# Kernel tuning notes

Measured on AMD Instinct MI355X. Metric: run time of the kernel, lower is better.

Reference implementation:

```python
import jax, jax.numpy as jnp
import numpy as np

BN_EPS = 1e-5
TAU = 1.0  # gumbel temperature

def setup_inputs() -> dict:
    key = jax.random.key(0)
    ks = jax.random.split(key, 6)
    B, O, F, H, HID = 32, 4096, 256, 8, 128
    x = jax.random.normal(ks[0], (B, O, F), dtype=jnp.float32)
    gumbel_noise = jax.random.gumbel(ks[1], (B, O, H), dtype=jnp.float32)
    W_in = jax.random.normal(ks[2], (F, HID), dtype=jnp.float32) * (1.0 / np.sqrt(F))
    b_in = jnp.zeros((HID,), jnp.float32)
    W_blk = jax.random.normal(ks[3], (HID, HID), dtype=jnp.float32) * (1.0 / np.sqrt(HID))
    b_blk = jnp.zeros((HID,), jnp.float32)
    bn_gamma = jnp.ones((HID,), jnp.float32)
    bn_beta = jnp.zeros((HID,), jnp.float32)
    W_fc = jax.random.normal(ks[4], (HID, H), dtype=jnp.float32) * (1.0 / np.sqrt(HID))
    b_fc = jnp.zeros((H,), jnp.float32)
    return {"x": x, "gumbel_noise": gumbel_noise, "W_in": W_in, "b_in": b_in,
            "W_blk": W_blk, "b_blk": b_blk, "bn_gamma": bn_gamma, "bn_beta": bn_beta,
            "W_fc": W_fc, "b_fc": b_fc}

def reference(x, gumbel_noise, W_in, b_in, W_blk, b_blk, bn_gamma, bn_beta, W_fc, b_fc):
    B, O, F = x.shape
    xf = x.reshape(B * O, F)
    # DynamicNetwork head: input linear + relu, one residual block (Linear+BN+ReLU), fc
    h = jax.nn.relu(xf @ W_in + b_in)  # (B*O, HID)
    z = h @ W_blk + b_blk
    mu = z.mean(axis=0)
    var = z.var(axis=0)  # biased var, matches BatchNorm training normalization
    z = (z - mu) * jax.lax.rsqrt(var + BN_EPS) * bn_gamma + bn_beta
    h = jax.nn.relu(z) + h  # residual
    logits = (h @ W_fc + b_fc).reshape(B, O, -1)  # (B, O, H)
    # mask out zero-norm observations
    mask = (jnp.linalg.norm(x, axis=2) != 0)[..., None].astype(x.dtype)  # (B, O, 1)
    logits = logits * mask
    # gumbel softmax over observation dim (soft)
    w = jax.nn.softmax((logits + gumbel_noise) / TAU, axis=1)  # (B, O, H)
    # weighted sum pooling: algebraically the repeat-multiply-sum in the original
    pooled = jnp.einsum('boh,bof->bhf', w, x)  # (B, H, F)
    return pooled.reshape(B, -1)  # (B, H*F)
```

## Files before the change

kernel.cpp:

```cpp
#include <hip/hip_runtime.h>
#include <hip/hip_bf16.h>
#include <math.h>

#define MB_ 131072
#define F_  256
#define HID_ 128
#define H_  8
#define O_  4096
#define B_  32

typedef __attribute__((ext_vector_type(8))) short short8;
typedef __attribute__((ext_vector_type(4))) float f32x4;

static __device__ __forceinline__ unsigned short f2bf(float f) {
    unsigned int u = __float_as_uint(f);
    unsigned int r = (u + 0x7fffu + ((u >> 16) & 1u)) >> 16;
    return (unsigned short)r;
}
static __device__ __forceinline__ float bf2f(unsigned short u) {
    return __uint_as_float(((unsigned int)u) << 16);
}
static __device__ __forceinline__ unsigned int pk2bf(float a, float b) {
    float2 f2; f2.x = a; f2.y = b;
    __hip_bfloat162 h = __float22bfloat162_rn(f2);
    union { __hip_bfloat162 h2; unsigned int u; } cv;
    cv.h2 = h;
    return cv.u;
}

__global__ __launch_bounds__(256) void k_prep(
    const float* __restrict__ W_in, const float* __restrict__ W_blk,
    unsigned short* __restrict__ Win_f, unsigned short* __restrict__ Wblk_f)
{
    const int idx = blockIdx.x * 256 + threadIdx.x;
    if (idx < 32768) {
        const int j = idx & 7, n = (idx >> 3) & 127, c = idx >> 10;
        Win_f[idx] = f2bf(W_in[(size_t)(c * 8 + j) * HID_ + n]);
    } else if (idx < 49152) {
        const int i2 = idx - 32768;
        const int j = i2 & 7, n = (i2 >> 3) & 127, c = i2 >> 10;
        Wblk_f[i2] = f2bf(W_blk[(size_t)(c * 8 + j) * HID_ + n]);
    }
}

__global__ __launch_bounds__(256, 3) void k_gemm1(
    const float* __restrict__ x, const unsigned short* __restrict__ Win_f,
    const float* __restrict__ b_in,
    unsigned short* __restrict__ h_f, float* __restrict__ mask_out)
{
    __shared__ __align__(16) unsigned short smem[128 * 136];
    unsigned short* a_s = smem;
    unsigned short* hb_s = smem;

    const int tid = threadIdx.x;
    const int R0 = blockIdx.x * 128;
    const int wave = tid >> 6;
    const int wrow = wave >> 1, wcol = wave & 1;
    const int lane = tid & 63;
    const int lm = lane & 15, quad = lane >> 4;
    const int srow = tid >> 3;
    const int sk = tid & 7;
    const int sq = sk >> 1, sh = sk & 1;

    f32x4 acc[4][4];
#pragma unroll
    for (int i = 0; i < 4; i++)
#pragma unroll
        for (int j = 0; j < 4; j++) acc[i][j] = (f32x4){0.f, 0.f, 0.f, 0.f};
    float ms[4] = {0.f, 0.f, 0.f, 0.f};

    const float* xrow = x + (size_t)(R0 + srow) * F_ + sk * 4;

    for (int kt = 0; kt < 8; kt++) {
#pragma unroll
        for (int p = 0; p < 4; p++) {
            const float4 v = *(const float4*)(xrow + kt * 32 + (size_t)(32 * p) * F_);
            ms[p] += v.x * v.x + v.y * v.y + v.z * v.z + v.w * v.w;
            uint2 w; w.x = pk2bf(v.x, v.y); w.y = pk2bf(v.z, v.w);
            *(uint2*)(&a_s[(sq * 132 + srow + 32 * p) * 8 + sh * 4]) = w;
        }
        __syncthreads();
        short8 af[4], bfr[4];
        const unsigned short* wf = Win_f + ((size_t)(kt * 4 + quad) * 128 + wcol * 64 + lm) * 8;
#pragma unroll
        for (int ni = 0; ni < 4; ni++)
            bfr[ni] = *(const short8*)(wf + ni * 16 * 8);
#pragma unroll
        for (int mi = 0; mi < 4; mi++)
            af[mi] = *(const short8*)(&a_s[(quad * 132 + wrow * 64 + mi * 16 + lm) * 8]);
#pragma unroll
        for (int mi = 0; mi < 4; mi++)
#pragma unroll
            for (int ni = 0; ni < 4; ni++)
                acc[mi][ni] = __builtin_amdgcn_mfma_f32_16x16x32_bf16(af[mi], bfr[ni], acc[mi][ni], 0, 0, 0);
        __syncthreads();
    }

#pragma unroll
    for (int p = 0; p < 4; p++) {
        float s = ms[p];
        s += __shfl_down(s, 4, 8);
        s += __shfl_down(s, 2, 8);
        s += __shfl_down(s, 1, 8);
        if (sk == 0) mask_out[R0 + srow + 32 * p] = (s != 0.f) ? 1.f : 0.f;
    }

    {
        float bcol[4];
#pragma unroll
        for (int ni = 0; ni < 4; ni++) bcol[ni] = b_in[wcol * 64 + ni * 16 + lm];
#pragma unroll
        for (int mi = 0; mi < 4; mi++)
#pragma unroll
            for (int r = 0; r < 4; r++) {
                const int row = wrow * 64 + mi * 16 + quad * 4 + r;
#pragma unroll
                for (int ni = 0; ni < 4; ni++) {
                    const int col = wcol * 64 + ni * 16 + lm;
                    hb_s[row * 136 + col] = f2bf(fmaxf(acc[mi][ni][r] + bcol[ni], 0.f));
                }
            }
    }
    __syncthreads();

    unsigned short* hf = h_f + (size_t)blockIdx.x * 16384;
#pragma unroll
    for (int i = 0; i < 8; i++) {
        const int idx = i * 256 + tid;
        const int c = idx >> 7, row = idx & 127;
        const short8 v = *(const short8*)(&hb_s[row * 136 + c * 8]);
        *(short8*)(hf + (size_t)idx * 8) = v;
    }
}

__global__ __launch_bounds__(256, 4) void k_gemm2stats(
    const unsigned short* __restrict__ h_f, const unsigned short* __restrict__ Wblk_f,
    const float* __restrict__ b_blk,
    float* __restrict__ sumP, float* __restrict__ sumsqP)
{
    __shared__ float csum_s[128], csumsq_s[128];
    const int tid = threadIdx.x;
    const int wave = tid >> 6;
    const int wrow = wave >> 1, wcol = wave & 1;
    const int lane = tid & 63;
    const int lm = lane & 15, quad = lane >> 4;

    if (tid < 128) { csum_s[tid] = 0.f; csumsq_s[tid] = 0.f; }
    __syncthreads();

    const unsigned short* hf = h_f + (size_t)blockIdx.x * 16384;

    f32x4 acc[4][4];
#pragma unroll
    for (int i = 0; i < 4; i++)
#pragma unroll
        for (int j = 0; j < 4; j++) acc[i][j] = (f32x4){0.f, 0.f, 0.f, 0.f};
#pragma unroll
    for (int kt = 0; kt < 4; kt++) {
        short8 af[4], bfr[4];
        const unsigned short* wf2 = Wblk_f + ((size_t)(kt * 4 + quad) * 128 + wcol * 64 + lm) * 8;
#pragma unroll
        for (int ni = 0; ni < 4; ni++)
            bfr[ni] = *(const short8*)(wf2 + ni * 16 * 8);
#pragma unroll
        for (int mi = 0; mi < 4; mi++)
            af[mi] = *(const short8*)(hf + ((size_t)(kt * 4 + quad) * 128 + wrow * 64 + mi * 16 + lm) * 8);
#pragma unroll
        for (int mi = 0; mi < 4; mi++)
#pragma unroll
            for (int ni = 0; ni < 4; ni++)
                acc[mi][ni] = __builtin_amdgcn_mfma_f32_16x16x32_bf16(af[mi], bfr[ni], acc[mi][ni], 0, 0, 0);
    }

    float bcol[4];
#pragma unroll
    for (int ni = 0; ni < 4; ni++) bcol[ni] = b_blk[wcol * 64 + ni * 16 + lm];
    float s_c[4] = {0.f, 0.f, 0.f, 0.f}, ss_c[4] = {0.f, 0.f, 0.f, 0.f};
#pragma unroll
    for (int mi = 0; mi < 4; mi++)
#pragma unroll
        for (int r = 0; r < 4; r++)
#pragma unroll
            for (int ni = 0; ni < 4; ni++) {
                const float zv = acc[mi][ni][r] + bcol[ni];
                s_c[ni] += zv;
                ss_c[ni] += zv * zv;
            }
#pragma unroll
    for (int ni = 0; ni < 4; ni++) {
        float s = s_c[ni], ss = ss_c[ni];
        s  += __shfl_xor(s, 16);  s  += __shfl_xor(s, 32);
        ss += __shfl_xor(ss, 16); ss += __shfl_xor(ss, 32);
        if (quad == 0) {
            atomicAdd(&csum_s[wcol * 64 + ni * 16 + lm], s);
            atomicAdd(&csumsq_s[wcol * 64 + ni * 16 + lm], ss);
        }
    }
    __syncthreads();
    if (tid < 128) {
        sumP[(size_t)blockIdx.x * 128 + tid] = csum_s[tid];
        sumsqP[(size_t)blockIdx.x * 128 + tid] = csumsq_s[tid];
    }
}

__global__ __launch_bounds__(256) void k_bnfin(
    const float* __restrict__ sumP, const float* __restrict__ sumsqP,
    const float* __restrict__ gamma, const float* __restrict__ beta,
    float* __restrict__ scale, float* __restrict__ shift)
{
    const int c = blockIdx.x;
    const int tid = threadIdx.x;
    float s = 0.f, ss = 0.f;
    for (int i = tid; i < 1024; i += 256) {
        s  += sumP[(size_t)i * 128 + c];
        ss += sumsqP[(size_t)i * 128 + c];
    }
#pragma unroll
    for (int off = 32; off; off >>= 1) {
        s  += __shfl_xor(s, off, 64);
        ss += __shfl_xor(ss, off, 64);
    }
    __shared__ float rs[4], rss[4];
    const int wid = tid >> 6, lane = tid & 63;
    if (lane == 0) { rs[wid] = s; rss[wid] = ss; }
    __syncthreads();
    if (tid == 0) {
        const float S  = rs[0] + rs[1] + rs[2] + rs[3];
        const float SS = rss[0] + rss[1] + rss[2] + rss[3];
        const float inv_m = 1.0f / (float)MB_;
        const float mu = S * inv_m;
        const float var = SS * inv_m - mu * mu;
        const float sc = gamma[c] * rsqrtf(var + 1e-5f);
        scale[c] = sc;
        shift[c] = beta[c] - mu * sc;
    }
}

__global__ __launch_bounds__(256, 3) void k_phaseC(
    const unsigned short* __restrict__ h_f, const unsigned short* __restrict__ Wblk_f,
    const float* __restrict__ b_blk,
    const float* __restrict__ scale, const float* __restrict__ shift,
    const float* __restrict__ W_fc, const float* __restrict__ b_fc,
    const float* __restrict__ mask, const float* __restrict__ gumbel,
    float* __restrict__ t_bho)
{
    __shared__ __align__(16) unsigned short hb_f[16384];
    __shared__ float wfc_s[128 * 8];
    __shared__ float sc_s[128], sh_s[128];

    const int tid = threadIdx.x;
    const int R0 = blockIdx.x * 128;
    const int wave = tid >> 6;
    const int wrow = wave >> 1, wcol = wave & 1;
    const int lane = tid & 63;
    const int lm = lane & 15, quad = lane >> 4;

    for (int i = tid; i < 1024; i += 256) wfc_s[i] = W_fc[i];
    if (tid < 128) { sc_s[tid] = scale[tid]; sh_s[tid] = shift[tid]; }
    const unsigned short* hf = h_f + (size_t)blockIdx.x * 16384;
#pragma unroll
    for (int i = 0; i < 8; i++) {
        const int idx = i * 256 + tid;
        const short8 v = *(const short8*)(hf + (size_t)idx * 8);
        *(short8*)(&hb_f[idx * 8]) = v;
    }
    __syncthreads();

    f32x4 acc[4][4];
#pragma unroll
    for (int i = 0; i < 4; i++)
#pragma unroll
        for (int j = 0; j < 4; j++) acc[i][j] = (f32x4){0.f, 0.f, 0.f, 0.f};
#pragma unroll
    for (int kt = 0; kt < 4; kt++) {
        short8 af[4], bfr[4];
        const unsigned short* wf2 = Wblk_f + ((size_t)(kt * 4 + quad) * 128 + wcol * 64 + lm) * 8;
#pragma unroll
        for (int ni = 0; ni < 4; ni++)
            bfr[ni] = *(const short8*)(wf2 + ni * 16 * 8);
#pragma unroll
        for (int mi = 0; mi < 4; mi++)
            af[mi] = *(const short8*)(&hb_f[((kt * 4 + quad) * 128 + wrow * 64 + mi * 16 + lm) * 8]);
#pragma unroll
        for (int mi = 0; mi < 4; mi++)
#pragma unroll
            for (int ni = 0; ni < 4; ni++)
                acc[mi][ni] = __builtin_amdgcn_mfma_f32_16x16x32_bf16(af[mi], bfr[ni], acc[mi][ni], 0, 0, 0);
    }
    __syncthreads();

    {
        float bcol[4];
#pragma unroll
        for (int ni = 0; ni < 4; ni++) bcol[ni] = b_blk[wcol * 64 + ni * 16 + lm];
#pragma unroll
        for (int mi = 0; mi < 4; mi++)
#pragma unroll
            for (int r = 0; r < 4; r++) {
                const int row = wrow * 64 + mi * 16 + quad * 4 + r;
#pragma unroll
                for (int ni = 0; ni < 4; ni++) {
                    const int col = wcol * 64 + ni * 16 + lm;
                    const int a = ((col >> 3) * 128 + row) * 8 + (col & 7);
                    const float zv = acc[mi][ni][r] + bcol[ni];
                    const float hv = bf2f(hb_f[a]);
                    hb_f[a] = f2bf(fmaxf(zv * sc_s[col] + sh_s[col], 0.f) + hv);
                }
            }
    }
    __syncthreads();

    {
        const int row = tid >> 1, half = tid & 1;
        const int grow = R0 + row;
        float a8[8];
#pragma unroll
        for (int j = 0; j < 8; j++) a8[j] = 0.f;
#pragma unroll 2
        for (int c8 = 0; c8 < 8; c8++) {
            const int c = half * 8 + c8;
            const short8 hv8 = *(const short8*)(&hb_f[(c * 128 + row) * 8]);
#pragma unroll
            for (int e = 0; e < 8; e++) {
                const float hv = bf2f((unsigned short)hv8[e]);
                const int k = c * 8 + e;
#pragma unroll
                for (int j = 0; j < 8; j++) a8[j] += hv * wfc_s[k * 8 + j];
            }
        }
#pragma unroll
        for (int j = 0; j < 8; j++) a8[j] += __shfl_xor(a8[j], 1);
        const float mk = mask[grow];
        const int b = grow >> 12, o = grow & 4095;
#pragma unroll
        for (int jj = 0; jj < 4; jj++) {
            const int j = half * 4 + jj;
            const float t = (a8[j] + b_fc[j]) * mk + gumbel[(size_t)grow * 8 + j];
            t_bho[((size_t)(b * 8 + j)) * O_ + o] = t;
        }
    }
}

__global__ __launch_bounds__(256) void k_softmax(
    const float* __restrict__ t_in, float* __restrict__ w_out)
{
    const int bh = blockIdx.x;
    const int tid = threadIdx.x;
    const float* tp = t_in + (size_t)bh * O_;
    float4 v[4];
    float mx = -3.4e38f;
#pragma unroll
    for (int it = 0; it < 4; it++) {
        v[it] = *(const float4*)(tp + it * 1024 + tid * 4);
        mx = fmaxf(mx, fmaxf(fmaxf(v[it].x, v[it].y), fmaxf(v[it].z, v[it].w)));
    }
#pragma unroll
    for (int off = 32; off; off >>= 1) mx = fmaxf(mx, __shfl_xor(mx, off, 64));
    __shared__ float rm[4], rsum[4];
    const int wid = tid >> 6, lane = tid & 63;
    if (lane == 0) rm[wid] = mx;
    __syncthreads();
    mx = fmaxf(fmaxf(rm[0], rm[1]), fmaxf(rm[2], rm[3]));
    float sum = 0.f;
#pragma unroll
    for (int it = 0; it < 4; it++) {
        v[it].x = __expf(v[it].x - mx); v[it].y = __expf(v[it].y - mx);
        v[it].z = __expf(v[it].z - mx); v[it].w = __expf(v[it].w - mx);
        sum += v[it].x + v[it].y + v[it].z + v[it].w;
    }
#pragma unroll
    for (int off = 32; off; off >>= 1) sum += __shfl_xor(sum, off, 64);
    if (lane == 0) rsum[wid] = sum;
    __syncthreads();
    sum = rsum[0] + rsum[1] + rsum[2] + rsum[3];
    const float inv = 1.f / sum;
    float* wp = w_out + (size_t)bh * O_;
#pragma unroll
    for (int it = 0; it < 4; it++) {
        float4 o;
        o.x = v[it].x * inv; o.y = v[it].y * inv; o.z = v[it].z * inv; o.w = v[it].w * inv;
        *(float4*)(wp + it * 1024 + tid * 4) = o;
    }
}

__global__ __launch_bounds__(256) void k_pool(
    const float* __restrict__ x, const float* __restrict__ w_in,
    float* __restrict__ pp)
{
    __shared__ float ws_s[8][128];
    const int tid = threadIdx.x;
    const int oc = blockIdx.x;
    const int b = blockIdx.y;
    const int wave = tid >> 6, lane = tid & 63;
    const int f = wave * 64 + lane;
    for (int i = tid; i < 1024; i += 256) {
        const int hh = i >> 7, oi = i & 127;
        ws_s[hh][oi] = w_in[((size_t)(b * 8 + hh)) * O_ + oc * 128 + oi];
    }
    __syncthreads();
    float acc[8];
#pragma unroll
    for (int hh = 0; hh < 8; hh++) acc[hh] = 0.f;
    const float* xp = x + ((size_t)(b * O_ + oc * 128)) * F_ + f;
#pragma unroll 1
    for (int oi = 0; oi < 128; oi += 4) {
        float xv[4];
#pragma unroll
        for (int u = 0; u < 4; u++) xv[u] = xp[(size_t)(oi + u) * F_];
#pragma unroll
        for (int u = 0; u < 4; u++)
#pragma unroll
            for (int hh = 0; hh < 8; hh++) acc[hh] += ws_s[hh][oi + u] * xv[u];
    }
    float* outp = pp + ((size_t)(oc * 32 + b)) * 2048;
#pragma unroll
    for (int hh = 0; hh < 8; hh++) outp[hh * 256 + f] = acc[hh];
}

__global__ __launch_bounds__(256) void k_reduce_pool(
    const float* __restrict__ pp, float* __restrict__ out)
{
    const size_t i = (size_t)blockIdx.x * 256 + threadIdx.x;
    float s = 0.f;
#pragma unroll
    for (int oc = 0; oc < 32; oc++) s += pp[(size_t)oc * 65536 + i];
    out[i] = s;
}

extern "C" void kernel_launch(void* const* d_in, const int* in_sizes, int n_in,
                              void* d_out, int out_size, void* d_ws, size_t ws_size,
                              hipStream_t stream)
{
    const float* x      = (const float*)d_in[0];
    const float* gumbel = (const float*)d_in[1];
    const float* W_in   = (const float*)d_in[2];
    const float* b_in   = (const float*)d_in[3];
    const float* W_blk  = (const float*)d_in[4];
    const float* b_blk  = (const float*)d_in[5];
    const float* gamma  = (const float*)d_in[6];
    const float* beta   = (const float*)d_in[7];
    const float* W_fc   = (const float*)d_in[8];
    const float* b_fc   = (const float*)d_in[9];
    float* out = (float*)d_out;
    char* ws = (char*)d_ws;

    unsigned short* h_f   = (unsigned short*)(ws + 0);
    float* mask   = (float*)(ws + 33554432);
    float* sumP   = (float*)(ws + 34078720);
    float* sumsqP = (float*)(ws + 34603008);
    float* scale  = (float*)(ws + 35127296);
    float* shift  = (float*)(ws + 35127808);
    float* t_buf  = (float*)(ws + 35128320);
    float* w_buf  = (float*)(ws + 39322624);
    float* pp     = (float*)(ws + 43516928);
    unsigned short* Win_f  = (unsigned short*)(ws + 51905536);
    unsigned short* Wblk_f = (unsigned short*)(ws + 51971072);

    k_prep<<<192, 256, 0, stream>>>(W_in, W_blk, Win_f, Wblk_f);
    k_gemm1<<<1024, 256, 0, stream>>>(x, Win_f, b_in, h_f, mask);
    k_gemm2stats<<<1024, 256, 0, stream>>>(h_f, Wblk_f, b_blk, sumP, sumsqP);
    k_bnfin<<<128, 256, 0, stream>>>(sumP, sumsqP, gamma, beta, scale, shift);
    k_phaseC<<<1024, 256, 0, stream>>>(h_f, Wblk_f, b_blk, scale, shift, W_fc, b_fc, mask, gumbel, t_buf);
    k_softmax<<<256, 256, 0, stream>>>(t_buf, w_buf);
    k_pool<<<dim3(32, 32), 256, 0, stream>>>(x, w_buf, pp);
    k_reduce_pool<<<256, 256, 0, stream>>>(pp, out);
}
```

Before: 316.3 us.

## Precast x to bf16, fuse gemm1 with gemm2 stats, pool from bf16 x

A new precast kernel converts x to bf16 once and computes the row mask. A fused kernel then loads a whole 128x256 bf16 tile into swizzled LDS, runs both GEMMs and the BN statistics without re-reading h from global memory. The pooling kernel now reads bf16 x instead of fp32, halving its input traffic. In exchange there is an extra full write and read of bf16 x, a 64KB LDS tile that lowers occupancy, and reduced pooling precision from using bf16 x in the weighted sum.

```diff
diff --git a/kernel.cpp b/kernel.cpp
--- a/kernel.cpp
+++ b/kernel.cpp
@@ -19,13 +19,6 @@
 }
 static __device__ __forceinline__ float bf2f(unsigned short u) {
     return __uint_as_float(((unsigned int)u) << 16);
-}
-static __device__ __forceinline__ unsigned int pk2bf(float a, float b) {
-    float2 f2; f2.x = a; f2.y = b;
-    __hip_bfloat162 h = __float22bfloat162_rn(f2);
-    union { __hip_bfloat162 h2; unsigned int u; } cv;
-    cv.h2 = h;
-    return cv.u;
 }
 
 __global__ __launch_bounds__(256) void k_prep(
@@ -43,14 +36,36 @@
     }
 }
 
-__global__ __launch_bounds__(256, 3) void k_gemm1(
-    const float* __restrict__ x, const unsigned short* __restrict__ Win_f,
-    const float* __restrict__ b_in,
-    unsigned short* __restrict__ h_f, float* __restrict__ mask_out)
-{
-    __shared__ __align__(16) unsigned short smem[128 * 136];
-    unsigned short* a_s = smem;
-    unsigned short* hb_s = smem;
+__global__ __launch_bounds__(256) void k_precast(
+    const float* __restrict__ x, unsigned short* __restrict__ xb,
+    float* __restrict__ mask_out)
+{
+    const int tid = threadIdx.x, wv = tid >> 6, ln = tid & 63;
+    const int rbase = blockIdx.x * 64;
+#pragma unroll 2
+    for (int it = 0; it < 16; it++) {
+        const int row = rbase + it * 4 + wv;
+        const float4 v = *(const float4*)(x + (size_t)row * F_ + ln * 4);
+        float ss = v.x * v.x + v.y * v.y + v.z * v.z + v.w * v.w;
+        ushort4 o;
+        o.x = f2bf(v.x); o.y = f2bf(v.y); o.z = f2bf(v.z); o.w = f2bf(v.w);
+        *(ushort4*)(xb + (size_t)row * F_ + ln * 4) = o;
+#pragma unroll
+        for (int off = 32; off; off >>= 1) ss += __shfl_xor(ss, off, 64);
+        if (ln == 0) mask_out[row] = (ss != 0.f) ? 1.f : 0.f;
+    }
+}
+
+__global__ __launch_bounds__(256, 2) void k_gemm1f(
+    const unsigned short* __restrict__ xb, const unsigned short* __restrict__ Win_f,
+    const unsigned short* __restrict__ Wblk_f,
+    const float* __restrict__ b_in, const float* __restrict__ b_blk,
+    unsigned short* __restrict__ h_f,
+    float* __restrict__ sumP, float* __restrict__ sumsqP)
+{
+    __shared__ __align__(16) unsigned short x_s[128 * 256];
+    __shared__ float csum_s[128], csumsq_s[128];
+    unsigned short* hb_s = x_s;
 
     const int tid = threadIdx.x;
     const int R0 = blockIdx.x * 128;
@@ -58,52 +73,48 @@
     const int wrow = wave >> 1, wcol = wave & 1;
     const int lane = tid & 63;
     const int lm = lane & 15, quad = lane >> 4;
-    const int srow = tid >> 3;
-    const int sk = tid & 7;
-    const int sq = sk >> 1, sh = sk & 1;
+
+    if (tid < 128) { csum_s[tid] = 0.f; csumsq_s[tid] = 0.f; }
+
+    {
+        const unsigned short* src = xb + (size_t)R0 * F_;
+#pragma unroll
+        for (int i = 0; i < 16; i++) {
+            const int idx = i * 256 + tid;
+            const int row = idx >> 5, c = idx & 31;
+            const int pc = c ^ (row & 7);
+            const short8 v = *(const short8*)(src + (size_t)idx * 8);
+            *(short8*)(&x_s[(row * 32 + pc) * 8]) = v;
+        }
+    }
+    __syncthreads();
 
     f32x4 acc[4][4];
 #pragma unroll
     for (int i = 0; i < 4; i++)
 #pragma unroll
         for (int j = 0; j < 4; j++) acc[i][j] = (f32x4){0.f, 0.f, 0.f, 0.f};
-    float ms[4] = {0.f, 0.f, 0.f, 0.f};
-
-    const float* xrow = x + (size_t)(R0 + srow) * F_ + sk * 4;
 
     for (int kt = 0; kt < 8; kt++) {
-#pragma unroll
-        for (int p = 0; p < 4; p++) {
-            const float4 v = *(const float4*)(xrow + kt * 32 + (size_t)(32 * p) * F_);
-            ms[p] += v.x * v.x + v.y * v.y + v.z * v.z + v.w * v.w;
-            uint2 w; w.x = pk2bf(v.x, v.y); w.y = pk2bf(v.z, v.w);
-            *(uint2*)(&a_s[(sq * 132 + srow + 32 * p) * 8 + sh * 4]) = w;
-        }
-        __syncthreads();
         short8 af[4], bfr[4];
         const unsigned short* wf = Win_f + ((size_t)(kt * 4 + quad) * 128 + wcol * 64 + lm) * 8;
 #pragma unroll
         for (int ni = 0; ni < 4; ni++)
             bfr[ni] = *(const short8*)(wf + ni * 16 * 8);
-#pragma unroll
-        for (int mi = 0; mi < 4; mi++)
-            af[mi] = *(const short8*)(&a_s[(quad * 132 + wrow * 64 + mi * 16 + lm) * 8]);
+        const int cidx = kt * 4 + quad;
+#pragma unroll
+        for (int mi = 0; mi < 4; mi++) {
+            const int row = wrow * 64 + mi * 16 + lm;
+            const int pc = cidx ^ (row & 7);
+            af[mi] = *(const short8*)(&x_s[(row * 32 + pc) * 8]);
+        }
 #pragma unroll
         for (int mi = 0; mi < 4; mi++)
 #pragma unroll
             for (int ni = 0; ni < 4; ni++)
                 acc[mi][ni] = __builtin_amdgcn_mfma_f32_16x16x32_bf16(af[mi], bfr[ni], acc[mi][ni], 0, 0, 0);
-        __syncthreads();
-    }
-
-#pragma unroll
-    for (int p = 0; p < 4; p++) {
-        float s = ms[p];
-        s += __shfl_down(s, 4, 8);
-        s += __shfl_down(s, 2, 8);
-        s += __shfl_down(s, 1, 8);
-        if (sk == 0) mask_out[R0 + srow + 32 * p] = (s != 0.f) ? 1.f : 0.f;
-    }
+    }
+    __syncthreads();
 
     {
         float bcol[4];
@@ -123,34 +134,17 @@
     }
     __syncthreads();
 
-    unsigned short* hf = h_f + (size_t)blockIdx.x * 16384;
-#pragma unroll
-    for (int i = 0; i < 8; i++) {
-        const int idx = i * 256 + tid;
-        const int c = idx >> 7, row = idx & 127;
-        const short8 v = *(const short8*)(&hb_s[row * 136 + c * 8]);
-        *(short8*)(hf + (size_t)idx * 8) = v;
-    }
-}
-
-__global__ __launch_bounds__(256, 4) void k_gemm2stats(
-    const unsigned short* __restrict__ h_f, const unsigned short* __restrict__ Wblk_f,
-    const float* __restrict__ b_blk,
-    float* __restrict__ sumP, float* __restrict__ sumsqP)
-{
-    __shared__ float csum_s[128], csumsq_s[128];
-    const int tid = threadIdx.x;
-    const int wave = tid >> 6;
-    const int wrow = wave >> 1, wcol = wave & 1;
-    const int lane = tid & 63;
-    const int lm = lane & 15, quad = lane >> 4;
-
-    if (tid < 128) { csum_s[tid] = 0.f; csumsq_s[tid] = 0.f; }
-    __syncthreads();
-
-    const unsigned short* hf = h_f + (size_t)blockIdx.x * 16384;
-
-    f32x4 acc[4][4];
+    {
+        unsigned short* hf = h_f + (size_t)blockIdx.x * 16384;
+#pragma unroll
+        for (int i = 0; i < 8; i++) {
+            const int idx = i * 256 + tid;
+            const int c = idx >> 7, row = idx & 127;
+            const short8 v = *(const short8*)(&hb_s[row * 136 + c * 8]);
+            *(short8*)(hf + (size_t)idx * 8) = v;
+        }
+    }
+
 #pragma unroll
     for (int i = 0; i < 4; i++)
 #pragma unroll
@@ -164,7 +158,7 @@
             bfr[ni] = *(const short8*)(wf2 + ni * 16 * 8);
 #pragma unroll
         for (int mi = 0; mi < 4; mi++)
-            af[mi] = *(const short8*)(hf + ((size_t)(kt * 4 + quad) * 128 + wrow * 64 + mi * 16 + lm) * 8);
+            af[mi] = *(const short8*)(&hb_s[(wrow * 64 + mi * 16 + lm) * 136 + kt * 32 + quad * 8]);
 #pragma unroll
         for (int mi = 0; mi < 4; mi++)
 #pragma unroll
@@ -172,28 +166,30 @@
                 acc[mi][ni] = __builtin_amdgcn_mfma_f32_16x16x32_bf16(af[mi], bfr[ni], acc[mi][ni], 0, 0, 0);
     }
 
-    float bcol[4];
-#pragma unroll
-    for (int ni = 0; ni < 4; ni++) bcol[ni] = b_blk[wcol * 64 + ni * 16 + lm];
-    float s_c[4] = {0.f, 0.f, 0.f, 0.f}, ss_c[4] = {0.f, 0.f, 0.f, 0.f};
-#pragma unroll
-    for (int mi = 0; mi < 4; mi++)
-#pragma unroll
-        for (int r = 0; r < 4; r++)
-#pragma unroll
-            for (int ni = 0; ni < 4; ni++) {
-                const float zv = acc[mi][ni][r] + bcol[ni];
-                s_c[ni] += zv;
-                ss_c[ni] += zv * zv;
+    {
+        float bcol[4];
+#pragma unroll
+        for (int ni = 0; ni < 4; ni++) bcol[ni] = b_blk[wcol * 64 + ni * 16 + lm];
+        float s_c[4] = {0.f, 0.f, 0.f, 0.f}, ss_c[4] = {0.f, 0.f, 0.f, 0.f};
+#pragma unroll
+        for (int mi = 0; mi < 4; mi++)
+#pragma unroll
+            for (int r = 0; r < 4; r++)
+#pragma unroll
+                for (int ni = 0; ni < 4; ni++) {
+                    const float zv = acc[mi][ni][r] + bcol[ni];
+                    s_c[ni] += zv;
+                    ss_c[ni] += zv * zv;
+                }
+#pragma unroll
+        for (int ni = 0; ni < 4; ni++) {
+            float s = s_c[ni], ss = ss_c[ni];
+            s  += __shfl_xor(s, 16);  s  += __shfl_xor(s, 32);
+            ss += __shfl_xor(ss, 16); ss += __shfl_xor(ss, 32);
+            if (quad == 0) {
+                atomicAdd(&csum_s[wcol * 64 + ni * 16 + lm], s);
+                atomicAdd(&csumsq_s[wcol * 64 + ni * 16 + lm], ss);
             }
-#pragma unroll
-    for (int ni = 0; ni < 4; ni++) {
-        float s = s_c[ni], ss = ss_c[ni];
-        s  += __shfl_xor(s, 16);  s  += __shfl_xor(s, 32);
-        ss += __shfl_xor(ss, 16); ss += __shfl_xor(ss, 32);
-        if (quad == 0) {
-            atomicAdd(&csum_s[wcol * 64 + ni * 16 + lm], s);
-            atomicAdd(&csumsq_s[wcol * 64 + ni * 16 + lm], ss);
         }
     }
     __syncthreads();
@@ -384,7 +380,7 @@
 }
 
 __global__ __launch_bounds__(256) void k_pool(
-    const float* __restrict__ x, const float* __restrict__ w_in,
+    const unsigned short* __restrict__ xb, const float* __restrict__ w_in,
     float* __restrict__ pp)
 {
     __shared__ float ws_s[8][128];
@@ -401,12 +397,12 @@
     float acc[8];
 #pragma unroll
     for (int hh = 0; hh < 8; hh++) acc[hh] = 0.f;
-    const float* xp = x + ((size_t)(b * O_ + oc * 128)) * F_ + f;
+    const unsigned short* xp = xb + ((size_t)(b * O_ + oc * 128)) * F_ + f;
 #pragma unroll 1
     for (int oi = 0; oi < 128; oi += 4) {
         float xv[4];
 #pragma unroll
-        for (int u = 0; u < 4; u++) xv[u] = xp[(size_t)(oi + u) * F_];
+        for (int u = 0; u < 4; u++) xv[u] = bf2f(xp[(size_t)(oi + u) * F_]);
 #pragma unroll
         for (int u = 0; u < 4; u++)
 #pragma unroll
@@ -444,24 +440,25 @@
     float* out = (float*)d_out;
     char* ws = (char*)d_ws;
 
-    unsigned short* h_f   = (unsigned short*)(ws + 0);
-    float* mask   = (float*)(ws + 33554432);
-    float* sumP   = (float*)(ws + 34078720);
-    float* sumsqP = (float*)(ws + 34603008);
-    float* scale  = (float*)(ws + 35127296);
-    float* shift  = (float*)(ws + 35127808);
-    float* t_buf  = (float*)(ws + 35128320);
-    float* w_buf  = (float*)(ws + 39322624);
-    float* pp     = (float*)(ws + 43516928);
-    unsigned short* Win_f  = (unsigned short*)(ws + 51905536);
-    unsigned short* Wblk_f = (unsigned short*)(ws + 51971072);
+    unsigned short* xb    = (unsigned short*)(ws + 0);
+    unsigned short* h_f   = (unsigned short*)(ws + 67108864);
+    float* mask   = (float*)(ws + 100663296);
+    float* sumP   = (float*)(ws + 101187584);
+    float* sumsqP = (float*)(ws + 101711872);
+    float* scale  = (float*)(ws + 102236160);
+    float* shift  = (float*)(ws + 102236672);
+    float* t_buf  = (float*)(ws + 102237184);
+    float* w_buf  = (float*)(ws + 106431488);
+    float* pp     = (float*)(ws + 110625792);
+    unsigned short* Win_f  = (unsigned short*)(ws + 119014400);
+    unsigned short* Wblk_f = (unsigned short*)(ws + 119079936);
 
     k_prep<<<192, 256, 0, stream>>>(W_in, W_blk, Win_f, Wblk_f);
-    k_gemm1<<<1024, 256, 0, stream>>>(x, Win_f, b_in, h_f, mask);
-    k_gemm2stats<<<1024, 256, 0, stream>>>(h_f, Wblk_f, b_blk, sumP, sumsqP);
+    k_precast<<<2048, 256, 0, stream>>>(x, xb, mask);
+    k_gemm1f<<<1024, 256, 0, stream>>>(xb, Win_f, Wblk_f, b_in, b_blk, h_f, sumP, sumsqP);
     k_bnfin<<<128, 256, 0, stream>>>(sumP, sumsqP, gamma, beta, scale, shift);
     k_phaseC<<<1024, 256, 0, stream>>>(h_f, Wblk_f, b_blk, scale, shift, W_fc, b_fc, mask, gumbel, t_buf);
     k_softmax<<<256, 256, 0, stream>>>(t_buf, w_buf);
-    k_pool<<<dim3(32, 32), 256, 0, stream>>>(x, w_buf, pp);
+    k_pool<<<dim3(32, 32), 256, 0, stream>>>(xb, w_buf, pp);
     k_reduce_pool<<<256, 256, 0, stream>>>(pp, out);
 }
```

After: 304.1 us. -3.9%, faster.
